# Optimization experiments

Measured on AMD Instinct MI355X. Metric: run time of the kernel, lower is better.

The kernel has to match this reference:

```python
import jax, jax.numpy as jnp
import numpy as np

B, T, D, H = 4, 2048, 1024, 16
S = D // H  # head dim

def setup_inputs() -> dict:
    key = jax.random.key(0)
    kx, kq, ku, kb = jax.random.split(key, 4)
    x = jax.random.normal(kx, (B, T, D), dtype=jnp.float32)
    # torch nn.Linear weights: (out, in); y = x @ W.T
    Wq = jax.random.normal(kq, (D, D), dtype=jnp.float32) * (1.0 / np.sqrt(D))
    Wu = jax.random.normal(ku, (D, D), dtype=jnp.float32) * (1.0 / np.sqrt(D))
    bu = jax.random.normal(kb, (D,), dtype=jnp.float32) * 0.01
    return {"x": x, "Wq": Wq, "Wu": Wu, "bu": bu}

def reference(x, Wq, Wu, bu):
    b, t, k = x.shape
    h, s = H, S
    # Bug in original module replicated: Q, K, V all use to_queries.
    q = x @ Wq.T  # (b,t,k)
    qh = q.reshape(b, t, h, s).transpose(0, 2, 1, 3)  # (b,h,t,s)
    scores = jnp.einsum('bhts,bhus->bhtu', qh, qh) / jnp.sqrt(jnp.asarray(s, x.dtype))
    w = jax.nn.softmax(scores, axis=-1)  # (b,h,t,t)
    out = jnp.einsum('bhtu,bhus->bhts', w, qh)  # (b,h,t,s)
    out = out.transpose(0, 2, 1, 3).reshape(b, t, k)  # merge heads
    return out @ Wu.T + bu
```

## Files before the change

### kernel.cpp

```cpp
#include <hip/hip_runtime.h>

#define B_ 4
#define T_ 2048
#define D_ 1024
#define H_ 16
#define S_ 64

typedef __attribute__((ext_vector_type(8))) short bf16x8;
typedef __attribute__((ext_vector_type(16))) float f32x16;
typedef unsigned int uint;

__device__ __forceinline__ short f2bf(float f) {
    union { float f; uint u; } v; v.f = f;
    uint r = v.u + 0x7fffu + ((v.u >> 16) & 1u);
    return (short)(r >> 16);
}

__device__ __forceinline__ void gld16(const short* g, short* l) {
    __builtin_amdgcn_global_load_lds((const __attribute__((address_space(1))) void*)g,
                                     (__attribute__((address_space(3))) void*)l, 16, 0, 0);
}

__global__ __launch_bounds__(256) void cvt3(const float* __restrict__ x,
                                            const float* __restrict__ wq,
                                            const float* __restrict__ wu,
                                            short* __restrict__ xb,
                                            short* __restrict__ wqb,
                                            short* __restrict__ wub) {
    const int NX = B_ * T_ * D_ / 8;
    const int NW = D_ * D_ / 8;
    int i = blockIdx.x * 256 + threadIdx.x;
    const float* src; short* dst; int off;
    if (i < NX)            { src = x;  dst = xb;  off = i; }
    else if (i < NX + NW)  { src = wq; dst = wqb; off = i - NX; }
    else                   { src = wu; dst = wub; off = i - NX - NW; }
    float4 a = *(const float4*)(src + (size_t)off * 8);
    float4 b = *(const float4*)(src + (size_t)off * 8 + 4);
    short o[8] = {f2bf(a.x), f2bf(a.y), f2bf(a.z), f2bf(a.w),
                  f2bf(b.x), f2bf(b.y), f2bf(b.z), f2bf(b.w)};
    *(bf16x8*)(dst + (size_t)off * 8) = *(bf16x8*)o;
}

template <bool OUT_BF16>
__global__ __launch_bounds__(256, 2) void gemm_bt(const short* __restrict__ A,
                                                  const short* __restrict__ Bt,
                                                  const float* __restrict__ bias,
                                                  void* __restrict__ Cv,
                                                  int M, int N, int K) {
    __shared__ short As[4096];
    __shared__ short Bs[4096];
    const int tid  = threadIdx.x;
    const int lane = tid & 63;
    const int wv   = tid >> 6;
    const int wm   = wv >> 1, wn = wv & 1;
    const int h32  = lane >> 5;
    const int m0 = blockIdx.y * 128, n0 = blockIdx.x * 128;
    const short* Ap = A + (size_t)m0 * K;
    const short* Bp = Bt + (size_t)n0 * K;

    f32x16 acc[2][2];
    #pragma unroll
    for (int i = 0; i < 2; ++i)
        #pragma unroll
        for (int j = 0; j < 2; ++j)
            #pragma unroll
            for (int r = 0; r < 16; ++r) acc[i][j][r] = 0.f;

    for (int k0 = 0; k0 < K; k0 += 32) {
        __syncthreads();
        gld16(Ap + (size_t)lane * K        + k0 + wv * 8, &As[(wv * 128) * 8]);
        gld16(Ap + (size_t)(64 + lane) * K + k0 + wv * 8, &As[(wv * 128 + 64) * 8]);
        gld16(Bp + (size_t)lane * K        + k0 + wv * 8, &Bs[(wv * 128) * 8]);
        gld16(Bp + (size_t)(64 + lane) * K + k0 + wv * 8, &Bs[(wv * 128 + 64) * 8]);
        __syncthreads();

        #pragma unroll
        for (int ks2 = 0; ks2 < 2; ++ks2) {
            const int kk8 = ks2 * 2 + h32;
            bf16x8 af[2], bfr[2];
            af[0]  = *(bf16x8*)&As[(kk8 * 128 + wm * 64 + (lane & 31)) * 8];
            af[1]  = *(bf16x8*)&As[(kk8 * 128 + wm * 64 + 32 + (lane & 31)) * 8];
            bfr[0] = *(bf16x8*)&Bs[(kk8 * 128 + wn * 64 + (lane & 31)) * 8];
            bfr[1] = *(bf16x8*)&Bs[(kk8 * 128 + wn * 64 + 32 + (lane & 31)) * 8];
            acc[0][0] = __builtin_amdgcn_mfma_f32_32x32x16_bf16(af[0], bfr[0], acc[0][0], 0, 0, 0);
            acc[0][1] = __builtin_amdgcn_mfma_f32_32x32x16_bf16(af[0], bfr[1], acc[0][1], 0, 0, 0);
            acc[1][0] = __builtin_amdgcn_mfma_f32_32x32x16_bf16(af[1], bfr[0], acc[1][0], 0, 0, 0);
            acc[1][1] = __builtin_amdgcn_mfma_f32_32x32x16_bf16(af[1], bfr[1], acc[1][1], 0, 0, 0);
        }
    }

    #pragma unroll
    for (int mt = 0; mt < 2; ++mt) {
        #pragma unroll
        for (int nt = 0; nt < 2; ++nt) {
            const int rbase = m0 + wm * 64 + mt * 32;
            const int col   = n0 + wn * 64 + nt * 32 + (lane & 31);
            float bv = 0.f;
            if (!OUT_BF16 && bias) bv = bias[col];
            #pragma unroll
            for (int r = 0; r < 16; ++r) {
                int row = rbase + (r & 3) + 8 * (r >> 2) + 4 * h32;
                if constexpr (OUT_BF16)
                    ((short*)Cv)[(size_t)row * N + col] = f2bf(acc[mt][nt][r]);
                else
                    ((float*)Cv)[(size_t)row * N + col] = acc[mt][nt][r] + bv;
            }
        }
    }
}

__global__ __launch_bounds__(256, 2) void attn_mfma(const short* __restrict__ q,
                                                    short* __restrict__ o) {
    __shared__ short smem[8192];
    const int tid  = threadIdx.x;
    const int lane = tid & 63;
    const int wv   = tid >> 6;
    const int h32  = lane >> 5;
    const int b  = blockIdx.y >> 4;
    const int hh = blockIdx.y & 15;
    const int t0 = blockIdx.x * 128;
    const short* qb = q + (size_t)b * (T_ * D_) + hh * S_;

    #pragma unroll
    for (int rep = 0; rep < 4; ++rep) {
        int f = rep * 256 + tid;
        int r = f >> 3, c8 = f & 7;
        bf16x8 v = *(const bf16x8*)(qb + (size_t)(t0 + r) * D_ + c8 * 8);
        *(bf16x8*)&smem[(c8 * 128 + (r ^ c8)) * 8] = v;
    }
    __syncthreads();
    bf16x8 Qreg[4];
    #pragma unroll
    for (int ks = 0; ks < 4; ++ks) {
        int kk8 = 2 * ks + h32;
        Qreg[ks] = *(bf16x8*)&smem[(kk8 * 128 + ((wv * 32 + (lane & 31)) ^ kk8)) * 8];
    }

    f32x16 accO0, accO1;
    #pragma unroll
    for (int i = 0; i < 16; ++i) { accO0[i] = 0.f; accO1[i] = 0.f; }
    float lsp = 0.f;
    const int prow16 = ((((lane & 7) << 2) | ((lane >> 3) & 3)) * 16) + h32 * 512;

    for (int u0 = 0; u0 < T_; u0 += 64) {
        __syncthreads();
        #pragma unroll
        for (int rep = 0; rep < 2; ++rep) {
            int f = rep * 256 + tid;
            int uu = f >> 3, c8 = f & 7;
            int u = (uu & 0x33) | ((uu & 4) << 1) | ((uu & 8) >> 1);
            bf16x8 v = *(const bf16x8*)(qb + (size_t)(u0 + u) * D_ + c8 * 8);
            *(bf16x8*)&smem[(c8 * 64 + (u ^ c8)) * 8] = v;
            short sv[8];
            *(bf16x8*)sv = v;
            int base = 4096 + (u >> 4) * 1024 + ((u >> 2) & 1) * 512 + (c8 >> 2) * 8
                     + ((u & 3) | (((u >> 3) & 1) << 2)) + (c8 & 3) * 16;
            #pragma unroll
            for (int ds = 0; ds < 8; ++ds)
                smem[base + ds * 64] = sv[ds];
        }
        __syncthreads();

        f32x16 aS0, aS1;
        #pragma unroll
        for (int i = 0; i < 16; ++i) { aS0[i] = 0.f; aS1[i] = 0.f; }
        #pragma unroll
        for (int ks = 0; ks < 4; ++ks) {
            int kk8 = 2 * ks + h32;
            bf16x8 k0 = *(bf16x8*)&smem[(kk8 * 64 + ((lane & 31) ^ kk8)) * 8];
            bf16x8 k1 = *(bf16x8*)&smem[(kk8 * 64 + ((32 + (lane & 31)) ^ kk8)) * 8];
            aS0 = __builtin_amdgcn_mfma_f32_32x32x16_bf16(k0, Qreg[ks], aS0, 0, 0, 0);
            aS1 = __builtin_amdgcn_mfma_f32_32x32x16_bf16(k1, Qreg[ks], aS1, 0, 0, 0);
        }

        bf16x8 af[4];
        #pragma unroll
        for (int tt = 0; tt < 2; ++tt) {
            const f32x16& a = tt ? aS1 : aS0;
            float p[16];
            #pragma unroll
            for (int r = 0; r < 16; ++r) { p[r] = __expf(a[r] * 0.125f); lsp += p[r]; }
            #pragma unroll
            for (int sub = 0; sub < 2; ++sub) {
                union { uint u[4]; bf16x8 v; } cv;
                #pragma unroll
                for (int dd = 0; dd < 4; ++dd)
                    cv.u[dd] = __builtin_amdgcn_perm(
                        __float_as_uint(p[sub * 8 + 2 * dd + 1]),
                        __float_as_uint(p[sub * 8 + 2 * dd]), 0x07060302u);
                af[tt * 2 + sub] = cv.v;
            }
        }

        #pragma unroll
        for (int c = 0; c < 4; ++c) {
            bf16x8 v0 = *(bf16x8*)&smem[4096 + c * 1024 + prow16 + 0];
            bf16x8 v1 = *(bf16x8*)&smem[4096 + c * 1024 + prow16 + 8];
            accO0 = __builtin_amdgcn_mfma_f32_32x32x16_bf16(af[c], v0, accO0, 0, 0, 0);
            accO1 = __builtin_amdgcn_mfma_f32_32x32x16_bf16(af[c], v1, accO1, 0, 0, 0);
        }
    }

    float dsum = lsp + __shfl_xor(lsp, 32);
    short* ob = o + (size_t)b * (T_ * D_) + hh * S_;
    #pragma unroll
    for (int r = 0; r < 16; ++r) {
        int rt = (r & 3) + 8 * (r >> 2) + 4 * h32;
        float inv = 1.00390625f / __shfl(dsum, rt);
        size_t t = (size_t)(t0 + wv * 32 + rt);
        ob[t * D_ + (lane & 31)]      = f2bf(accO0[r] * inv);
        ob[t * D_ + 32 + (lane & 31)] = f2bf(accO1[r] * inv);
    }
}

extern "C" void kernel_launch(void* const* d_in, const int* in_sizes, int n_in,
                              void* d_out, int out_size, void* d_ws, size_t ws_size,
                              hipStream_t stream) {
    const float* x  = (const float*)d_in[0];
    const float* Wq = (const float*)d_in[1];
    const float* Wu = (const float*)d_in[2];
    const float* bu = (const float*)d_in[3];
    float* out  = (float*)d_out;
    short* qbuf = (short*)d_out;
    short* xb   = (short*)((char*)d_out + 16777216);
    short* attn = (short*)d_ws;
    short* wqb  = (short*)((char*)d_ws + 16777216);
    short* wub  = (short*)((char*)d_ws + 18874368);

    const int M = B_ * T_;
    dim3 blk(256);
    dim3 gg(D_ / 128, M / 128);
    hipLaunchKernelGGL(cvt3, dim3(5120), blk, 0, stream, x, Wq, Wu, xb, wqb, wub);
    hipLaunchKernelGGL((gemm_bt<true>), gg, blk, 0, stream,
                       xb, wqb, (const float*)nullptr, (void*)qbuf, M, D_, D_);
    hipLaunchKernelGGL(attn_mfma, dim3(T_ / 128, B_ * H_), blk, 0, stream, qbuf, attn);
    hipLaunchKernelGGL((gemm_bt<false>), gg, blk, 0, stream,
                       attn, wub, bu, (void*)out, M, D_, D_);
}
```

Baseline: 256.6 us.

## Triple-buffer GEMM LDS staging and double-buffer K/V tiles in attention

The GEMM now keeps three LDS stages filled by async global-to-LDS loads, gated by explicit vmcnt waits and raw barriers, so global fetches overlap the MFMA work instead of stalling on every k-step. The attention kernel prefetches the next K/V tile into registers and writes it into a second LDS buffer while the current tile is being consumed, which removes one barrier per iteration. This raises LDS use (triple buffers in the GEMM, doubled smem in attention), which may lower occupancy, and relies on hand-placed waitcnt and barriers being correct.

```diff
diff --git a/kernel.cpp b/kernel.cpp
--- a/kernel.cpp
+++ b/kernel.cpp
@@ -41,14 +41,22 @@
     *(bf16x8*)(dst + (size_t)off * 8) = *(bf16x8*)o;
 }
 
+#define STAGE_G(t, bi) do {                                                       \
+        int kk_ = (t) << 5;                                                       \
+        gld16(Ap + (size_t)lane * K        + kk_ + wv * 8, &As[bi][(wv * 128) * 8]);      \
+        gld16(Ap + (size_t)(64 + lane) * K + kk_ + wv * 8, &As[bi][(wv * 128 + 64) * 8]); \
+        gld16(Bp + (size_t)lane * K        + kk_ + wv * 8, &Bs[bi][(wv * 128) * 8]);      \
+        gld16(Bp + (size_t)(64 + lane) * K + kk_ + wv * 8, &Bs[bi][(wv * 128 + 64) * 8]); \
+    } while (0)
+
 template <bool OUT_BF16>
 __global__ __launch_bounds__(256, 2) void gemm_bt(const short* __restrict__ A,
                                                   const short* __restrict__ Bt,
                                                   const float* __restrict__ bias,
                                                   void* __restrict__ Cv,
                                                   int M, int N, int K) {
-    __shared__ short As[4096];
-    __shared__ short Bs[4096];
+    __shared__ short As[3][4096];
+    __shared__ short Bs[3][4096];
     const int tid  = threadIdx.x;
     const int lane = tid & 63;
     const int wv   = tid >> 6;
@@ -66,44 +74,55 @@
             #pragma unroll
             for (int r = 0; r < 16; ++r) acc[i][j][r] = 0.f;
 
-    for (int k0 = 0; k0 < K; k0 += 32) {
-        __syncthreads();
-        gld16(Ap + (size_t)lane * K        + k0 + wv * 8, &As[(wv * 128) * 8]);
-        gld16(Ap + (size_t)(64 + lane) * K + k0 + wv * 8, &As[(wv * 128 + 64) * 8]);
-        gld16(Bp + (size_t)lane * K        + k0 + wv * 8, &Bs[(wv * 128) * 8]);
-        gld16(Bp + (size_t)(64 + lane) * K + k0 + wv * 8, &Bs[(wv * 128 + 64) * 8]);
-        __syncthreads();
-
+    const int nt = K >> 5;
+    STAGE_G(0, 0);
+    STAGE_G(1, 1);
+    STAGE_G(2, 2);
+
+    int bi = 0;
+    for (int t = 0; t < nt; ++t) {
+        if (t + 2 < nt)      asm volatile("s_waitcnt vmcnt(8)" ::: "memory");
+        else if (t + 1 < nt) asm volatile("s_waitcnt vmcnt(4)" ::: "memory");
+        else                 asm volatile("s_waitcnt vmcnt(0)" ::: "memory");
+        __builtin_amdgcn_s_barrier();
+        asm volatile("" ::: "memory");
+
+        const short* Ab = As[bi];
+        const short* Bb = Bs[bi];
         #pragma unroll
         for (int ks2 = 0; ks2 < 2; ++ks2) {
             const int kk8 = ks2 * 2 + h32;
-            bf16x8 af[2], bfr[2];
-            af[0]  = *(bf16x8*)&As[(kk8 * 128 + wm * 64 + (lane & 31)) * 8];
-            af[1]  = *(bf16x8*)&As[(kk8 * 128 + wm * 64 + 32 + (lane & 31)) * 8];
-            bfr[0] = *(bf16x8*)&Bs[(kk8 * 128 + wn * 64 + (lane & 31)) * 8];
-            bfr[1] = *(bf16x8*)&Bs[(kk8 * 128 + wn * 64 + 32 + (lane & 31)) * 8];
-            acc[0][0] = __builtin_amdgcn_mfma_f32_32x32x16_bf16(af[0], bfr[0], acc[0][0], 0, 0, 0);
-            acc[0][1] = __builtin_amdgcn_mfma_f32_32x32x16_bf16(af[0], bfr[1], acc[0][1], 0, 0, 0);
-            acc[1][0] = __builtin_amdgcn_mfma_f32_32x32x16_bf16(af[1], bfr[0], acc[1][0], 0, 0, 0);
-            acc[1][1] = __builtin_amdgcn_mfma_f32_32x32x16_bf16(af[1], bfr[1], acc[1][1], 0, 0, 0);
-        }
+            bf16x8 af0  = *(bf16x8*)&Ab[(kk8 * 128 + wm * 64 + (lane & 31)) * 8];
+            bf16x8 af1  = *(bf16x8*)&Ab[(kk8 * 128 + wm * 64 + 32 + (lane & 31)) * 8];
+            bf16x8 bfr0 = *(bf16x8*)&Bb[(kk8 * 128 + wn * 64 + (lane & 31)) * 8];
+            bf16x8 bfr1 = *(bf16x8*)&Bb[(kk8 * 128 + wn * 64 + 32 + (lane & 31)) * 8];
+            acc[0][0] = __builtin_amdgcn_mfma_f32_32x32x16_bf16(af0, bfr0, acc[0][0], 0, 0, 0);
+            acc[0][1] = __builtin_amdgcn_mfma_f32_32x32x16_bf16(af0, bfr1, acc[0][1], 0, 0, 0);
+            acc[1][0] = __builtin_amdgcn_mfma_f32_32x32x16_bf16(af1, bfr0, acc[1][0], 0, 0, 0);
+            acc[1][1] = __builtin_amdgcn_mfma_f32_32x32x16_bf16(af1, bfr1, acc[1][1], 0, 0, 0);
+        }
+
+        asm volatile("" ::: "memory");
+        __builtin_amdgcn_s_barrier();
+        if (t + 3 < nt) STAGE_G(t + 3, bi);
+        bi = (bi == 2) ? 0 : bi + 1;
     }
 
     #pragma unroll
     for (int mt = 0; mt < 2; ++mt) {
         #pragma unroll
-        for (int nt = 0; nt < 2; ++nt) {
+        for (int nt2 = 0; nt2 < 2; ++nt2) {
             const int rbase = m0 + wm * 64 + mt * 32;
-            const int col   = n0 + wn * 64 + nt * 32 + (lane & 31);
+            const int col   = n0 + wn * 64 + nt2 * 32 + (lane & 31);
             float bv = 0.f;
             if (!OUT_BF16 && bias) bv = bias[col];
             #pragma unroll
             for (int r = 0; r < 16; ++r) {
                 int row = rbase + (r & 3) + 8 * (r >> 2) + 4 * h32;
                 if constexpr (OUT_BF16)
-                    ((short*)Cv)[(size_t)row * N + col] = f2bf(acc[mt][nt][r]);
+                    ((short*)Cv)[(size_t)row * N + col] = f2bf(acc[mt][nt2][r]);
                 else
-                    ((float*)Cv)[(size_t)row * N + col] = acc[mt][nt][r] + bv;
+                    ((float*)Cv)[(size_t)row * N + col] = acc[mt][nt2][r] + bv;
             }
         }
     }
@@ -111,7 +130,7 @@
 
 __global__ __launch_bounds__(256, 2) void attn_mfma(const short* __restrict__ q,
                                                     short* __restrict__ o) {
-    __shared__ short smem[8192];
+    __shared__ short smem[16384];
     const int tid  = threadIdx.x;
     const int lane = tid & 63;
     const int wv   = tid >> 6;
@@ -121,12 +140,28 @@
     const int t0 = blockIdx.x * 128;
     const short* qb = q + (size_t)b * (T_ * D_) + hh * S_;
 
+    const int c8  = tid & 7;
+    const int uu0 = tid >> 3;
+    const int uu1 = uu0 + 32;
+    const int u_0 = (uu0 & 0x33) | ((uu0 & 4) << 1) | ((uu0 & 8) >> 1);
+    const int u_1 = (uu1 & 0x33) | ((uu1 & 4) << 1) | ((uu1 & 8) >> 1);
+    const int kfo0 = (c8 * 64 + (u_0 ^ c8)) * 8;
+    const int kfo1 = (c8 * 64 + (u_1 ^ c8)) * 8;
+    const int kto0 = 4096 + (u_0 >> 4) * 1024 + ((u_0 >> 2) & 1) * 512 + (c8 >> 2) * 8
+                   + ((u_0 & 3) | (((u_0 >> 3) & 1) << 2)) + (c8 & 3) * 16;
+    const int kto1 = 4096 + (u_1 >> 4) * 1024 + ((u_1 >> 2) & 1) * 512 + (c8 >> 2) * 8
+                   + ((u_1 & 3) | (((u_1 >> 3) & 1) << 2)) + (c8 & 3) * 16;
+    const short* g0 = qb + (size_t)u_0 * D_ + c8 * 8;
+    const short* g1 = qb + (size_t)u_1 * D_ + c8 * 8;
+
+    bf16x8 st0 = *(const bf16x8*)g0;
+    bf16x8 st1 = *(const bf16x8*)g1;
     #pragma unroll
     for (int rep = 0; rep < 4; ++rep) {
         int f = rep * 256 + tid;
-        int r = f >> 3, c8 = f & 7;
-        bf16x8 v = *(const bf16x8*)(qb + (size_t)(t0 + r) * D_ + c8 * 8);
-        *(bf16x8*)&smem[(c8 * 128 + (r ^ c8)) * 8] = v;
+        int r = f >> 3, cq = f & 7;
+        bf16x8 v = *(const bf16x8*)(qb + (size_t)(t0 + r) * D_ + cq * 8);
+        *(bf16x8*)&smem[(cq * 128 + (r ^ cq)) * 8] = v;
     }
     __syncthreads();
     bf16x8 Qreg[4];
@@ -135,6 +170,16 @@
         int kk8 = 2 * ks + h32;
         Qreg[ks] = *(bf16x8*)&smem[(kk8 * 128 + ((wv * 32 + (lane & 31)) ^ kk8)) * 8];
     }
+    __syncthreads();
+    *(bf16x8*)&smem[kfo0] = st0;
+    *(bf16x8*)&smem[kfo1] = st1;
+    #pragma unroll
+    for (int ds = 0; ds < 8; ++ds) {
+        smem[kto0 + ds * 64] = st0[ds];
+        smem[kto1 + ds * 64] = st1[ds];
+    }
+    st0 = *(const bf16x8*)(g0 + (size_t)64 * D_);
+    st1 = *(const bf16x8*)(g1 + (size_t)64 * D_);
 
     f32x16 accO0, accO1;
     #pragma unroll
@@ -142,24 +187,10 @@
     float lsp = 0.f;
     const int prow16 = ((((lane & 7) << 2) | ((lane >> 3) & 3)) * 16) + h32 * 512;
 
+    int rb = 0;
     for (int u0 = 0; u0 < T_; u0 += 64) {
         __syncthreads();
-        #pragma unroll
-        for (int rep = 0; rep < 2; ++rep) {
-            int f = rep * 256 + tid;
-            int uu = f >> 3, c8 = f & 7;
-            int u = (uu & 0x33) | ((uu & 4) << 1) | ((uu & 8) >> 1);
-            bf16x8 v = *(const bf16x8*)(qb + (size_t)(u0 + u) * D_ + c8 * 8);
-            *(bf16x8*)&smem[(c8 * 64 + (u ^ c8)) * 8] = v;
-            short sv[8];
-            *(bf16x8*)sv = v;
-            int base = 4096 + (u >> 4) * 1024 + ((u >> 2) & 1) * 512 + (c8 >> 2) * 8
-                     + ((u & 3) | (((u >> 3) & 1) << 2)) + (c8 & 3) * 16;
-            #pragma unroll
-            for (int ds = 0; ds < 8; ++ds)
-                smem[base + ds * 64] = sv[ds];
-        }
-        __syncthreads();
+        const int wb = rb ^ 8192;
 
         f32x16 aS0, aS1;
         #pragma unroll
@@ -167,11 +198,22 @@
         #pragma unroll
         for (int ks = 0; ks < 4; ++ks) {
             int kk8 = 2 * ks + h32;
-            bf16x8 k0 = *(bf16x8*)&smem[(kk8 * 64 + ((lane & 31) ^ kk8)) * 8];
-            bf16x8 k1 = *(bf16x8*)&smem[(kk8 * 64 + ((32 + (lane & 31)) ^ kk8)) * 8];
+            bf16x8 k0 = *(bf16x8*)&smem[rb + (kk8 * 64 + ((lane & 31) ^ kk8)) * 8];
+            bf16x8 k1 = *(bf16x8*)&smem[rb + (kk8 * 64 + ((32 + (lane & 31)) ^ kk8)) * 8];
             aS0 = __builtin_amdgcn_mfma_f32_32x32x16_bf16(k0, Qreg[ks], aS0, 0, 0, 0);
             aS1 = __builtin_amdgcn_mfma_f32_32x32x16_bf16(k1, Qreg[ks], aS1, 0, 0, 0);
         }
+
+        *(bf16x8*)&smem[wb + kfo0] = st0;
+        *(bf16x8*)&smem[wb + kfo1] = st1;
+        #pragma unroll
+        for (int ds = 0; ds < 8; ++ds) {
+            smem[wb + kto0 + ds * 64] = st0[ds];
+            smem[wb + kto1 + ds * 64] = st1[ds];
+        }
+        int un = u0 + 128; if (un >= T_) un = 0;
+        st0 = *(const bf16x8*)(g0 + (size_t)un * D_);
+        st1 = *(const bf16x8*)(g1 + (size_t)un * D_);
 
         bf16x8 af[4];
         #pragma unroll
@@ -194,11 +236,12 @@
 
         #pragma unroll
         for (int c = 0; c < 4; ++c) {
-            bf16x8 v0 = *(bf16x8*)&smem[4096 + c * 1024 + prow16 + 0];
-            bf16x8 v1 = *(bf16x8*)&smem[4096 + c * 1024 + prow16 + 8];
+            bf16x8 v0 = *(bf16x8*)&smem[rb + 4096 + c * 1024 + prow16 + 0];
+            bf16x8 v1 = *(bf16x8*)&smem[rb + 4096 + c * 1024 + prow16 + 8];
             accO0 = __builtin_amdgcn_mfma_f32_32x32x16_bf16(af[c], v0, accO0, 0, 0, 0);
             accO1 = __builtin_amdgcn_mfma_f32_32x32x16_bf16(af[c], v1, accO1, 0, 0, 0);
         }
+        rb = wb;
     }
 
     float dsum = lsp + __shfl_xor(lsp, 32);
```

Measured after the change: 254.9 us. No clear change (-0.7%).
